# Kernel tuning notes

Hardware: AMD Instinct MI355X
Metric: run time of the kernel (lower is better)

## Reference

```python
import jax, jax.numpy as jnp
import numpy as np


def _maxpool2x2(x):
    # x: [B, C, H, W] -> [B, C, H//2, W//2], 2x2 max pool stride 2
    B, C, H, W = x.shape
    return x.reshape(B, C, H // 2, 2, W // 2, 2).max(axis=(3, 5))


def _conv1x1(w, x):
    # w: [O, I], x: [B, I, H, W] -> [B, O, H, W]
    return jnp.einsum('oi,bihw->bohw', w, x)


def setup_inputs() -> dict:
    key = jax.random.key(0)
    ks = jax.random.split(key, 5)
    B, C, H, W = 16, 64, 64, 64
    c8, c2 = C // 8, C // 2
    x = jax.random.normal(ks[0], (B, C, H, W), dtype=jnp.float32)
    # 1x1 conv weights (spectral_norm is a training-time weight reparameterization;
    # here we use the effective weights directly, scaled for stability)
    w_theta = jax.random.normal(ks[1], (c8, C), dtype=jnp.float32) / np.sqrt(C)
    w_phi = jax.random.normal(ks[2], (c8, C), dtype=jnp.float32) / np.sqrt(C)
    w_g = jax.random.normal(ks[3], (c2, C), dtype=jnp.float32) / np.sqrt(C)
    w_o = jax.random.normal(ks[4], (C, c2), dtype=jnp.float32) / np.sqrt(c2)
    gamma = jnp.ones((1,), dtype=jnp.float32)
    return {"x": x, "w_theta": w_theta, "w_phi": w_phi, "w_g": w_g, "w_o": w_o, "gamma": gamma}


def reference(x, w_theta, w_phi, w_g, w_o, gamma):
    B, C, H, W = x.shape
    c8, c2 = C // 8, C // 2
    hw, hw4 = H * W, (H * W) // 4
    theta = _conv1x1(w_theta, x).reshape(B, c8, hw)            # [B, c8, hw]
    phi = _maxpool2x2(_conv1x1(w_phi, x)).reshape(B, c8, hw4)   # [B, c8, hw/4]
    attn = jax.nn.softmax(jnp.einsum('bcq,bck->bqk', theta, phi), axis=-1)  # [B, hw, hw/4]
    g = _maxpool2x2(_conv1x1(w_g, x)).reshape(B, c2, hw4)       # [B, c2, hw/4]
    attn_g = jnp.einsum('bck,bqk->bcq', g, attn).reshape(B, c2, H, W)
    out = x + gamma * _conv1x1(w_o, attn_g)
    return out
```

## Files before the change

### kernel.cpp

```cpp
#include <hip/hip_runtime.h>
#include <hip/hip_bf16.h>

#define B_  16
#define C_  64
#define HW  4096
#define KP  1024
#define LOG2E 1.44269504088896f

typedef short short8 __attribute__((ext_vector_type(8)));
typedef float floatx16 __attribute__((ext_vector_type(16)));

union Frag { uint4 u; short8 s; };

#define G_ROW      2064
#define ATTN_ROW   144
#define UNION_SZ   73728
#define WO_OFF     UNION_SZ
#define WO_ROW     80
#define L_OFF      (WO_OFF + 5120)
#define LDS_BYTES  (L_OFF + 2048)

__device__ __forceinline__ unsigned cvt_pk_bf16(float lo, float hi) {
    unsigned r;
    asm("v_cvt_pk_bf16_f32 %0, %1, %2" : "=v"(r) : "v"(lo), "v"(hi));
    return r;
}
#define PLSWAP(a, b) asm("v_permlane32_swap_b32 %0, %1" : "+v"(a), "+v"(b))

__device__ __forceinline__ void build_pfrags(const float* p, Frag& f0, Frag& f1) {
    unsigned u0 = cvt_pk_bf16(p[0], p[1]);
    unsigned u1 = cvt_pk_bf16(p[2], p[3]);
    unsigned u2 = cvt_pk_bf16(p[4], p[5]);
    unsigned u3 = cvt_pk_bf16(p[6], p[7]);
    PLSWAP(u0, u2);
    PLSWAP(u1, u3);
    f0.u.x = u0; f0.u.y = u1; f0.u.z = u2; f0.u.w = u3;
    unsigned v0 = cvt_pk_bf16(p[8],  p[9]);
    unsigned v1 = cvt_pk_bf16(p[10], p[11]);
    unsigned v2 = cvt_pk_bf16(p[12], p[13]);
    unsigned v3 = cvt_pk_bf16(p[14], p[15]);
    PLSWAP(v0, v2);
    PLSWAP(v1, v3);
    f1.u.x = v0; f1.u.y = v1; f1.u.z = v2; f1.u.w = v3;
}

__global__ __launch_bounds__(128) void convpool_kernel(
    const float* __restrict__ x,
    const float* __restrict__ w_theta,
    const float* __restrict__ w_phi,
    const float* __restrict__ w_g,
    __hip_bfloat16* __restrict__ theta16,
    __hip_bfloat16* __restrict__ phi16,
    __hip_bfloat16* __restrict__ gT)
{
    __shared__ float conv[48 * 129];
    const int bi = blockIdx.x;
    const int b  = bi >> 5;
    const int rg = bi & 31;
    const int t  = threadIdx.x;
    const int q  = rg * 128 + t;

    const float* xp = x + (size_t)b * C_ * HW + q;

    const int lane = t & 63;
    const int ln   = lane & 31;
    const int hi   = lane >> 5;
    const int wv   = t >> 6;

    const float* wrow0 = (ln < 8)  ? (w_theta + ln * C_)
                       : (ln < 16) ? (w_phi + (ln - 8) * C_)
                                   : (w_g + (ln - 16) * C_);
    const float* wrow1 = (ln < 16) ? (w_g + (16 + ln) * C_) : (w_g + 31 * C_);

    Frag B0[4], B1[4];
    #pragma unroll
    for (int k = 0; k < 4; ++k) {
        const float* p0 = wrow0 + 16 * k + 8 * hi;
        const float4 f0 = *(const float4*)(p0);
        const float4 f1 = *(const float4*)(p0 + 4);
        B0[k].u.x = cvt_pk_bf16(f0.x, f0.y); B0[k].u.y = cvt_pk_bf16(f0.z, f0.w);
        B0[k].u.z = cvt_pk_bf16(f1.x, f1.y); B0[k].u.w = cvt_pk_bf16(f1.z, f1.w);
        const float* p1 = wrow1 + 16 * k + 8 * hi;
        const float4 g0 = *(const float4*)(p1);
        const float4 g1 = *(const float4*)(p1 + 4);
        B1[k].u.x = cvt_pk_bf16(g0.x, g0.y); B1[k].u.y = cvt_pk_bf16(g0.z, g0.w);
        B1[k].u.z = cvt_pk_bf16(g1.x, g1.y); B1[k].u.w = cvt_pk_bf16(g1.z, g1.w);
    }

    floatx16 D00 = {}, D01 = {}, D10 = {}, D11 = {};

#define CHUNK(BUF, KK)                                                          \
    {                                                                           \
        unsigned q0 = cvt_pk_bf16(BUF[0],  BUF[1]);                             \
        unsigned q1 = cvt_pk_bf16(BUF[2],  BUF[3]);                             \
        unsigned q2 = cvt_pk_bf16(BUF[4],  BUF[5]);                             \
        unsigned q3 = cvt_pk_bf16(BUF[6],  BUF[7]);                             \
        unsigned q4 = cvt_pk_bf16(BUF[8],  BUF[9]);                             \
        unsigned q5 = cvt_pk_bf16(BUF[10], BUF[11]);                            \
        unsigned q6 = cvt_pk_bf16(BUF[12], BUF[13]);                            \
        unsigned q7 = cvt_pk_bf16(BUF[14], BUF[15]);                            \
        PLSWAP(q0, q4); PLSWAP(q1, q5); PLSWAP(q2, q6); PLSWAP(q3, q7);         \
        Frag loF, hiF;                                                          \
        loF.u.x = q0; loF.u.y = q1; loF.u.z = q2; loF.u.w = q3;                 \
        hiF.u.x = q4; hiF.u.y = q5; hiF.u.z = q6; hiF.u.w = q7;                 \
        D00 = __builtin_amdgcn_mfma_f32_32x32x16_bf16(loF.s, B0[KK].s, D00, 0, 0, 0); \
        D01 = __builtin_amdgcn_mfma_f32_32x32x16_bf16(loF.s, B1[KK].s, D01, 0, 0, 0); \
        D10 = __builtin_amdgcn_mfma_f32_32x32x16_bf16(hiF.s, B0[KK].s, D10, 0, 0, 0); \
        D11 = __builtin_amdgcn_mfma_f32_32x32x16_bf16(hiF.s, B1[KK].s, D11, 0, 0, 0); \
    }

    float xa[16], xc[16];
    #pragma unroll
    for (int c = 0; c < 16; ++c) xa[c] = xp[(size_t)c * HW];
    #pragma unroll
    for (int c = 0; c < 16; ++c) xc[c] = xp[(size_t)(16 + c) * HW];
    CHUNK(xa, 0);
    #pragma unroll
    for (int c = 0; c < 16; ++c) xa[c] = xp[(size_t)(32 + c) * HW];
    CHUNK(xc, 1);
    #pragma unroll
    for (int c = 0; c < 16; ++c) xc[c] = xp[(size_t)(48 + c) * HW];
    CHUNK(xa, 2);
    CHUNK(xc, 3);
#undef CHUNK

    #pragma unroll
    for (int rI = 0; rI < 16; ++rI) {
        const int row = (rI & 3) + 8 * (rI >> 2) + 4 * hi;
        conv[ln * 129 + (wv * 64 + row)]      = D00[rI];
        conv[ln * 129 + (wv * 64 + 32 + row)] = D10[rI];
        if (ln < 16) {
            conv[(32 + ln) * 129 + (wv * 64 + row)]      = D01[rI];
            conv[(32 + ln) * 129 + (wv * 64 + 32 + row)] = D11[rI];
        }
    }
    __syncthreads();

    {
        float th[8];
        #pragma unroll
        for (int oc = 0; oc < 8; ++oc) th[oc] = conv[oc * 129 + t] * LOG2E;
        uint4 u, z = {0u, 0u, 0u, 0u};
        u.x = cvt_pk_bf16(th[0], th[1]);
        u.y = cvt_pk_bf16(th[2], th[3]);
        u.z = cvt_pk_bf16(th[4], th[5]);
        u.w = cvt_pk_bf16(th[6], th[7]);
        __hip_bfloat16* tp = theta16 + ((size_t)b * HW + q) * 16;
        *(uint4*)(tp)     = u;
        *(uint4*)(tp + 8) = z;
    }

    for (int wi = t; wi < 40 * 32; wi += 128) {
        const int oc = (wi >> 5) + 8;
        const int pc = wi & 31;
        const int i00 = pc * 2;
        const float* cp = conv + oc * 129;
        const float v = fmaxf(fmaxf(cp[i00], cp[i00 + 1]),
                              fmaxf(cp[i00 + 64], cp[i00 + 65]));
        const int kg = rg * 32 + pc;
        if (oc < 16) phi16[((size_t)b * KP + kg) * 16 + (oc - 8)] = __float2bfloat16(v);
        else         gT[((size_t)b * 32 + (oc - 16)) * KP + kg]   = __float2bfloat16(v);
    }
    if (t < 32) {
        uint4 z = {0u, 0u, 0u, 0u};
        *(uint4*)(phi16 + ((size_t)b * KP + rg * 32 + t) * 16 + 8) = z;
    }
}

__global__ __launch_bounds__(512, 2) void attn_kernel(
    const float* __restrict__ x,
    const float* __restrict__ w_o,
    const float* __restrict__ gamma_p,
    const __hip_bfloat16* __restrict__ theta16,
    const __hip_bfloat16* __restrict__ phi16,
    const __hip_bfloat16* __restrict__ gT,
    float* __restrict__ out)
{
    __shared__ __align__(16) char lds[LDS_BYTES];
    const int t = threadIdx.x;
    const int bid = (blockIdx.x & 7) * 32 + (blockIdx.x >> 3);
    const int b   = bid >> 4;
    const int qb0 = (bid & 15) * 256;

    {
        const uint4* src = (const uint4*)(gT + (size_t)b * 32 * KP);
        #pragma unroll
        for (int i = 0; i < 8; ++i) {
            const int gi = t + 512 * i;
            const int c = gi >> 7, kk = gi & 127;
            *(uint4*)(lds + c * G_ROW + kk * 16) = src[gi];
        }
    }
    if (t < 256) {
        const int co = t >> 2, part = t & 3;
        const float4* wsrc = (const float4*)(w_o + co * 32 + part * 8);
        const float4 f0 = wsrc[0], f1 = wsrc[1];
        uint4 u;
        u.x = cvt_pk_bf16(f0.x, f0.y); u.y = cvt_pk_bf16(f0.z, f0.w);
        u.z = cvt_pk_bf16(f1.x, f1.y); u.w = cvt_pk_bf16(f1.z, f1.w);
        *(uint4*)(lds + WO_OFF + co * WO_ROW + part * 16) = u;
    }
    __syncthreads();

    const int lane = t & 63;
    const int wv   = t >> 6;
    const int h    = wv >> 2;
    const int qp   = wv & 3;
    const int hi   = lane >> 5;
    const int ln   = lane & 31;
    const int qt0  = qp * 64, qt1 = qt0 + 32;
    const int kbase = h * 512;

    const uint4* thb = (const uint4*)(theta16 + ((size_t)b * HW + qb0) * 16);
    Frag bth0, bth1;
    bth0.u = thb[(qt0 + ln) * 2 + hi];
    bth1.u = thb[(qt1 + ln) * 2 + hi];

    const uint4* phb = (const uint4*)(phi16 + ((size_t)b * KP + kbase) * 16);
    const char*  gp  = lds + ln * G_ROW + kbase * 2 + hi * 16;

    floatx16 czero = {};
    floatx16 O0 = {}, O1 = {};
    float l0 = 0.f, l1 = 0.f;

    #pragma unroll 2
    for (int kb = 0; kb < 16; ++kb) {
        Frag aphi, gf0, gf1;
        aphi.u = phb[(kb * 32 + ln) * 2 + hi];
        gf0.u  = *(const uint4*)(gp + kb * 64);
        gf1.u  = *(const uint4*)(gp + kb * 64 + 32);

        floatx16 S0 = __builtin_amdgcn_mfma_f32_32x32x16_bf16(aphi.s, bth0.s, czero, 0, 0, 0);
        floatx16 S1 = __builtin_amdgcn_mfma_f32_32x32x16_bf16(aphi.s, bth1.s, czero, 0, 0, 0);

        float p0[16], p1[16];
        float la = 0.f, lb = 0.f, lc = 0.f, ld = 0.f;
        #pragma unroll
        for (int rr = 0; rr < 16; rr += 2) {
            p0[rr]   = __builtin_amdgcn_exp2f(S0[rr]);   la += p0[rr];
            p0[rr+1] = __builtin_amdgcn_exp2f(S0[rr+1]); lb += p0[rr+1];
        }
        #pragma unroll
        for (int rr = 0; rr < 16; rr += 2) {
            p1[rr]   = __builtin_amdgcn_exp2f(S1[rr]);   lc += p1[rr];
            p1[rr+1] = __builtin_amdgcn_exp2f(S1[rr+1]); ld += p1[rr+1];
        }
        l0 += la + lb; l1 += lc + ld;

        Frag pa00, pa01, pa10, pa11;
        build_pfrags(p0, pa00, pa01);
        build_pfrags(p1, pa10, pa11);

        O0 = __builtin_amdgcn_mfma_f32_32x32x16_bf16(pa00.s, gf0.s, O0, 0, 0, 0);
        O0 = __builtin_amdgcn_mfma_f32_32x32x16_bf16(pa01.s, gf1.s, O0, 0, 0, 0);
        O1 = __builtin_amdgcn_mfma_f32_32x32x16_bf16(pa10.s, gf0.s, O1, 0, 0, 0);
        O1 = __builtin_amdgcn_mfma_f32_32x32x16_bf16(pa11.s, gf1.s, O1, 0, 0, 0);
    }

    __syncthreads();

    #pragma unroll
    for (int rr = 0; rr < 16; ++rr) {
        const int rm = (rr & 3) + 8 * (rr >> 2) + 4 * hi;
        *(float*)(lds + ((h << 8) + qt0 + rm) * ATTN_ROW + ln * 4) = O0[rr];
        *(float*)(lds + ((h << 8) + qt1 + rm) * ATTN_ROW + ln * 4) = O1[rr];
    }
    const float l0t = l0 + __shfl_xor(l0, 32, 64);
    const float l1t = l1 + __shfl_xor(l1, 32, 64);
    {
        const int   lq = hi ? (qt1 + ln) : (qt0 + ln);
        const float lw = hi ? l1t : l0t;
        *(float*)(lds + L_OFF + ((h << 8) + lq) * 4) = lw;
    }
    __syncthreads();

    const float gam = gamma_p[0];
    const int   qt  = wv * 32;
    const float lt  = *(const float*)(lds + L_OFF + (qt + ln) * 4)
                    + *(const float*)(lds + L_OFF + (256 + qt + ln) * 4);
    const float gl  = gam / lt;

    const char* ab0 = lds + (qt + ln) * ATTN_ROW + hi * 32;
    const char* ab1 = ab0 + 256 * ATTN_ROW;
    float4 a0 = *(const float4*)(ab0);
    float4 a1 = *(const float4*)(ab0 + 16);
    float4 a2 = *(const float4*)(ab0 + 64);
    float4 a3 = *(const float4*)(ab0 + 80);
    const float4 c0 = *(const float4*)(ab1);
    const float4 c1 = *(const float4*)(ab1 + 16);
    const float4 c2 = *(const float4*)(ab1 + 64);
    const float4 c3 = *(const float4*)(ab1 + 80);
    a0.x += c0.x; a0.y += c0.y; a0.z += c0.z; a0.w += c0.w;
    a1.x += c1.x; a1.y += c1.y; a1.z += c1.z; a1.w += c1.w;
    a2.x += c2.x; a2.y += c2.y; a2.z += c2.z; a2.w += c2.w;
    a3.x += c3.x; a3.y += c3.y; a3.z += c3.z; a3.w += c3.w;

    Frag bat0, bat1;
    bat0.u.x = cvt_pk_bf16(a0.x, a0.y); bat0.u.y = cvt_pk_bf16(a0.z, a0.w);
    bat0.u.z = cvt_pk_bf16(a1.x, a1.y); bat0.u.w = cvt_pk_bf16(a1.z, a1.w);
    bat1.u.x = cvt_pk_bf16(a2.x, a2.y); bat1.u.y = cvt_pk_bf16(a2.z, a2.w);
    bat1.u.z = cvt_pk_bf16(a3.x, a3.y); bat1.u.w = cvt_pk_bf16(a3.z, a3.w);

    const char* wb = lds + WO_OFF + ln * WO_ROW + hi * 16;
    Frag wa00, wa01, wa10, wa11;
    wa00.u = *(const uint4*)(wb);
    wa01.u = *(const uint4*)(wb + 32);
    wa10.u = *(const uint4*)(wb + 32 * WO_ROW);
    wa11.u = *(const uint4*)(wb + 32 * WO_ROW + 32);

    floatx16 D0 = __builtin_amdgcn_mfma_f32_32x32x16_bf16(wa00.s, bat0.s, czero, 0, 0, 0);
    D0 = __builtin_amdgcn_mfma_f32_32x32x16_bf16(wa01.s, bat1.s, D0, 0, 0, 0);
    floatx16 D1 = __builtin_amdgcn_mfma_f32_32x32x16_bf16(wa10.s, bat0.s, czero, 0, 0, 0);
    D1 = __builtin_amdgcn_mfma_f32_32x32x16_bf16(wa11.s, bat1.s, D1, 0, 0, 0);

    const int qg = qb0 + qt + ln;
    const float* xb = x   + (size_t)b * C_ * HW + qg;
    float*       ob = out + (size_t)b * C_ * HW + qg;
    #pragma unroll
    for (int rr = 0; rr < 16; ++rr) {
        const int co = (rr & 3) + 8 * (rr >> 2) + 4 * hi;
        ob[(size_t)co * HW]        = xb[(size_t)co * HW]        + gl * D0[rr];
        ob[(size_t)(co + 32) * HW] = xb[(size_t)(co + 32) * HW] + gl * D1[rr];
    }
}

extern "C" void kernel_launch(void* const* d_in, const int* in_sizes, int n_in,
                              void* d_out, int out_size, void* d_ws, size_t ws_size,
                              hipStream_t stream) {
    const float* x       = (const float*)d_in[0];
    const float* w_theta = (const float*)d_in[1];
    const float* w_phi   = (const float*)d_in[2];
    const float* w_g     = (const float*)d_in[3];
    const float* w_o     = (const float*)d_in[4];
    const float* gamma   = (const float*)d_in[5];
    float* out = (float*)d_out;

    __hip_bfloat16* theta16 = (__hip_bfloat16*)d_ws;
    __hip_bfloat16* phi16   = theta16 + (size_t)B_ * HW * 16;
    __hip_bfloat16* gT      = phi16   + (size_t)B_ * KP * 16;

    convpool_kernel<<<dim3(B_ * 32), dim3(128), 0, stream>>>(
        x, w_theta, w_phi, w_g, theta16, phi16, gT);
    attn_kernel<<<dim3(B_ * 16), dim3(512), 0, stream>>>(
        x, w_o, gamma, theta16, phi16, gT, out);
}
```

Baseline: 31.45 us.

## Split conv input channels across waves and shrink attention tiles for more blocks

The conv kernel now uses 256 threads, stages x tiles through LDS with coalesced float4 loads, and splits the 64 input channels between two wave halves, summing the partial results in LDS. The attention kernel moves from 256 blocks of 512 threads handling 256 queries each to 1024 blocks of 256 threads handling 64 queries each. It reads g directly from global memory instead of staging it in LDS and stages theta in LDS. The aim is higher occupancy and better load balance across the CUs, at the cost of redundant phi/g reads per block and an output epilogue that only half the waves run.

```diff
diff --git a/kernel.cpp b/kernel.cpp
--- a/kernel.cpp
+++ b/kernel.cpp
@@ -11,14 +11,6 @@
 typedef float floatx16 __attribute__((ext_vector_type(16)));
 
 union Frag { uint4 u; short8 s; };
-
-#define G_ROW      2064
-#define ATTN_ROW   144
-#define UNION_SZ   73728
-#define WO_OFF     UNION_SZ
-#define WO_ROW     80
-#define L_OFF      (WO_OFF + 5120)
-#define LDS_BYTES  (L_OFF + 2048)
 
 __device__ __forceinline__ unsigned cvt_pk_bf16(float lo, float hi) {
     unsigned r;
@@ -44,7 +36,12 @@
     f1.u.x = v0; f1.u.y = v1; f1.u.z = v2; f1.u.w = v3;
 }
 
-__global__ __launch_bounds__(128) void convpool_kernel(
+#define XS_ROW   528
+#define CV_ROW2  532
+#define CV_HALF  25536
+#define CLDS_SZ  51072
+
+__global__ __launch_bounds__(256) void convpool_kernel(
     const float* __restrict__ x,
     const float* __restrict__ w_theta,
     const float* __restrict__ w_phi,
@@ -53,110 +50,121 @@
     __hip_bfloat16* __restrict__ phi16,
     __hip_bfloat16* __restrict__ gT)
 {
-    __shared__ float conv[48 * 129];
+    __shared__ __align__(16) char clds[CLDS_SZ];
     const int bi = blockIdx.x;
     const int b  = bi >> 5;
     const int rg = bi & 31;
     const int t  = threadIdx.x;
-    const int q  = rg * 128 + t;
-
-    const float* xp = x + (size_t)b * C_ * HW + q;
 
     const int lane = t & 63;
     const int ln   = lane & 31;
     const int hi   = lane >> 5;
     const int wv   = t >> 6;
+    const int half = wv >> 1;
+    const int pt   = wv & 1;
+
+    {
+        const float* xsrc = x + (size_t)b * C_ * HW + rg * 128;
+        #pragma unroll
+        for (int i = 0; i < 8; ++i) {
+            const int idx = t + 256 * i;
+            const int c = idx >> 5, p4 = (idx & 31) * 4;
+            const float4 v = *(const float4*)(xsrc + (size_t)c * HW + p4);
+            *(float4*)(clds + c * XS_ROW + p4 * 4) = v;
+        }
+    }
 
     const float* wrow0 = (ln < 8)  ? (w_theta + ln * C_)
                        : (ln < 16) ? (w_phi + (ln - 8) * C_)
                                    : (w_g + (ln - 16) * C_);
     const float* wrow1 = (ln < 16) ? (w_g + (16 + ln) * C_) : (w_g + 31 * C_);
-
-    Frag B0[4], B1[4];
+    Frag B0[2], B1[2];
     #pragma unroll
-    for (int k = 0; k < 4; ++k) {
-        const float* p0 = wrow0 + 16 * k + 8 * hi;
+    for (int k = 0; k < 2; ++k) {
+        const float* p0 = wrow0 + 32 * half + 16 * k + 8 * hi;
         const float4 f0 = *(const float4*)(p0);
         const float4 f1 = *(const float4*)(p0 + 4);
         B0[k].u.x = cvt_pk_bf16(f0.x, f0.y); B0[k].u.y = cvt_pk_bf16(f0.z, f0.w);
         B0[k].u.z = cvt_pk_bf16(f1.x, f1.y); B0[k].u.w = cvt_pk_bf16(f1.z, f1.w);
-        const float* p1 = wrow1 + 16 * k + 8 * hi;
+        const float* p1 = wrow1 + 32 * half + 16 * k + 8 * hi;
         const float4 g0 = *(const float4*)(p1);
         const float4 g1 = *(const float4*)(p1 + 4);
         B1[k].u.x = cvt_pk_bf16(g0.x, g0.y); B1[k].u.y = cvt_pk_bf16(g0.z, g0.w);
         B1[k].u.z = cvt_pk_bf16(g1.x, g1.y); B1[k].u.w = cvt_pk_bf16(g1.z, g1.w);
     }
+    __syncthreads();
+
+    const int px = pt * 64 + lane;
+    Frag AL[2], AH[2];
+    #pragma unroll
+    for (int k = 0; k < 2; ++k) {
+        float v[16];
+        #pragma unroll
+        for (int j = 0; j < 16; ++j)
+            v[j] = *(const float*)(clds + (32 * half + 16 * k + j) * XS_ROW + px * 4);
+        unsigned q0 = cvt_pk_bf16(v[0],  v[1]);
+        unsigned q1 = cvt_pk_bf16(v[2],  v[3]);
+        unsigned q2 = cvt_pk_bf16(v[4],  v[5]);
+        unsigned q3 = cvt_pk_bf16(v[6],  v[7]);
+        unsigned q4 = cvt_pk_bf16(v[8],  v[9]);
+        unsigned q5 = cvt_pk_bf16(v[10], v[11]);
+        unsigned q6 = cvt_pk_bf16(v[12], v[13]);
+        unsigned q7 = cvt_pk_bf16(v[14], v[15]);
+        PLSWAP(q0, q4); PLSWAP(q1, q5); PLSWAP(q2, q6); PLSWAP(q3, q7);
+        AL[k].u.x = q0; AL[k].u.y = q1; AL[k].u.z = q2; AL[k].u.w = q3;
+        AH[k].u.x = q4; AH[k].u.y = q5; AH[k].u.z = q6; AH[k].u.w = q7;
+    }
+    __syncthreads();
 
     floatx16 D00 = {}, D01 = {}, D10 = {}, D11 = {};
-
-#define CHUNK(BUF, KK)                                                          \
-    {                                                                           \
-        unsigned q0 = cvt_pk_bf16(BUF[0],  BUF[1]);                             \
-        unsigned q1 = cvt_pk_bf16(BUF[2],  BUF[3]);                             \
-        unsigned q2 = cvt_pk_bf16(BUF[4],  BUF[5]);                             \
-        unsigned q3 = cvt_pk_bf16(BUF[6],  BUF[7]);                             \
-        unsigned q4 = cvt_pk_bf16(BUF[8],  BUF[9]);                             \
-        unsigned q5 = cvt_pk_bf16(BUF[10], BUF[11]);                            \
-        unsigned q6 = cvt_pk_bf16(BUF[12], BUF[13]);                            \
-        unsigned q7 = cvt_pk_bf16(BUF[14], BUF[15]);                            \
-        PLSWAP(q0, q4); PLSWAP(q1, q5); PLSWAP(q2, q6); PLSWAP(q3, q7);         \
-        Frag loF, hiF;                                                          \
-        loF.u.x = q0; loF.u.y = q1; loF.u.z = q2; loF.u.w = q3;                 \
-        hiF.u.x = q4; hiF.u.y = q5; hiF.u.z = q6; hiF.u.w = q7;                 \
-        D00 = __builtin_amdgcn_mfma_f32_32x32x16_bf16(loF.s, B0[KK].s, D00, 0, 0, 0); \
-        D01 = __builtin_amdgcn_mfma_f32_32x32x16_bf16(loF.s, B1[KK].s, D01, 0, 0, 0); \
-        D10 = __builtin_amdgcn_mfma_f32_32x32x16_bf16(hiF.s, B0[KK].s, D10, 0, 0, 0); \
-        D11 = __builtin_amdgcn_mfma_f32_32x32x16_bf16(hiF.s, B1[KK].s, D11, 0, 0, 0); \
-    }
-
-    float xa[16], xc[16];
     #pragma unroll
-    for (int c = 0; c < 16; ++c) xa[c] = xp[(size_t)c * HW];
-    #pragma unroll
-    for (int c = 0; c < 16; ++c) xc[c] = xp[(size_t)(16 + c) * HW];
-    CHUNK(xa, 0);
-    #pragma unroll
-    for (int c = 0; c < 16; ++c) xa[c] = xp[(size_t)(32 + c) * HW];
-    CHUNK(xc, 1);
-    #pragma unroll
-    for (int c = 0; c < 16; ++c) xc[c] = xp[(size_t)(48 + c) * HW];
-    CHUNK(xa, 2);
-    CHUNK(xc, 3);
-#undef CHUNK
-
-    #pragma unroll
-    for (int rI = 0; rI < 16; ++rI) {
-        const int row = (rI & 3) + 8 * (rI >> 2) + 4 * hi;
-        conv[ln * 129 + (wv * 64 + row)]      = D00[rI];
-        conv[ln * 129 + (wv * 64 + 32 + row)] = D10[rI];
-        if (ln < 16) {
-            conv[(32 + ln) * 129 + (wv * 64 + row)]      = D01[rI];
-            conv[(32 + ln) * 129 + (wv * 64 + 32 + row)] = D11[rI];
+    for (int k = 0; k < 2; ++k) {
+        D00 = __builtin_amdgcn_mfma_f32_32x32x16_bf16(AL[k].s, B0[k].s, D00, 0, 0, 0);
+        D01 = __builtin_amdgcn_mfma_f32_32x32x16_bf16(AL[k].s, B1[k].s, D01, 0, 0, 0);
+        D10 = __builtin_amdgcn_mfma_f32_32x32x16_bf16(AH[k].s, B0[k].s, D10, 0, 0, 0);
+        D11 = __builtin_amdgcn_mfma_f32_32x32x16_bf16(AH[k].s, B1[k].s, D11, 0, 0, 0);
+    }
+
+    {
+        char* base = clds + half * CV_HALF;
+        #pragma unroll
+        for (int r = 0; r < 16; ++r) {
+            const int row = (r & 3) + 8 * (r >> 2) + 4 * hi;
+            *(float*)(base + ln * CV_ROW2 + (pt * 64 + row) * 4)      = D00[r];
+            *(float*)(base + ln * CV_ROW2 + (pt * 64 + 32 + row) * 4) = D10[r];
+            if (ln < 16) {
+                *(float*)(base + (32 + ln) * CV_ROW2 + (pt * 64 + row) * 4)      = D01[r];
+                *(float*)(base + (32 + ln) * CV_ROW2 + (pt * 64 + 32 + row) * 4) = D11[r];
+            }
         }
     }
     __syncthreads();
 
-    {
+    if (t < 128) {
         float th[8];
         #pragma unroll
-        for (int oc = 0; oc < 8; ++oc) th[oc] = conv[oc * 129 + t] * LOG2E;
-        uint4 u, z = {0u, 0u, 0u, 0u};
-        u.x = cvt_pk_bf16(th[0], th[1]);
-        u.y = cvt_pk_bf16(th[2], th[3]);
-        u.z = cvt_pk_bf16(th[4], th[5]);
-        u.w = cvt_pk_bf16(th[6], th[7]);
-        __hip_bfloat16* tp = theta16 + ((size_t)b * HW + q) * 16;
+        for (int oc = 0; oc < 8; ++oc)
+            th[oc] = (*(const float*)(clds + oc * CV_ROW2 + t * 4)
+                    + *(const float*)(clds + CV_HALF + oc * CV_ROW2 + t * 4)) * LOG2E;
+        uint4 u; uint4 z = {0u, 0u, 0u, 0u};
+        u.x = cvt_pk_bf16(th[0], th[1]); u.y = cvt_pk_bf16(th[2], th[3]);
+        u.z = cvt_pk_bf16(th[4], th[5]); u.w = cvt_pk_bf16(th[6], th[7]);
+        __hip_bfloat16* tp = theta16 + ((size_t)b * HW + rg * 128 + t) * 16;
         *(uint4*)(tp)     = u;
         *(uint4*)(tp + 8) = z;
     }
 
-    for (int wi = t; wi < 40 * 32; wi += 128) {
+    for (int wi = t; wi < 1280; wi += 256) {
         const int oc = (wi >> 5) + 8;
         const int pc = wi & 31;
-        const int i00 = pc * 2;
-        const float* cp = conv + oc * 129;
-        const float v = fmaxf(fmaxf(cp[i00], cp[i00 + 1]),
-                              fmaxf(cp[i00 + 64], cp[i00 + 65]));
+        const char* c0 = clds + oc * CV_ROW2;
+        const char* c1 = clds + CV_HALF + oc * CV_ROW2;
+        const int i0 = pc * 8;
+        const float v00 = *(const float*)(c0 + i0)       + *(const float*)(c1 + i0);
+        const float v01 = *(const float*)(c0 + i0 + 4)   + *(const float*)(c1 + i0 + 4);
+        const float v10 = *(const float*)(c0 + i0 + 256) + *(const float*)(c1 + i0 + 256);
+        const float v11 = *(const float*)(c0 + i0 + 260) + *(const float*)(c1 + i0 + 260);
+        const float v = fmaxf(fmaxf(v00, v01), fmaxf(v10, v11));
         const int kg = rg * 32 + pc;
         if (oc < 16) phi16[((size_t)b * KP + kg) * 16 + (oc - 8)] = __float2bfloat16(v);
         else         gT[((size_t)b * 32 + (oc - 16)) * KP + kg]   = __float2bfloat16(v);
@@ -167,7 +175,15 @@
     }
 }
 
-__global__ __launch_bounds__(512, 2) void attn_kernel(
+#define AT_OFF   0
+#define AT_ROW   144
+#define AL_OFF   18432
+#define TH2_OFF  18944
+#define WO2_OFF  20992
+#define WO_ROW   80
+#define ALDS_SZ  26112
+
+__global__ __launch_bounds__(256, 4) void attn_kernel(
     const float* __restrict__ x,
     const float* __restrict__ w_o,
     const float* __restrict__ gamma_p,
@@ -176,52 +192,45 @@
     const __hip_bfloat16* __restrict__ gT,
     float* __restrict__ out)
 {
-    __shared__ __align__(16) char lds[LDS_BYTES];
+    __shared__ __align__(16) char lds[ALDS_SZ];
     const int t = threadIdx.x;
-    const int bid = (blockIdx.x & 7) * 32 + (blockIdx.x >> 3);
-    const int b   = bid >> 4;
-    const int qb0 = (bid & 15) * 256;
-
+    const int xcd = blockIdx.x & 7, slot = blockIdx.x >> 3;
+    const int b   = xcd * 2 + (slot >> 6);
+    const int qb0 = (slot & 63) * 64;
+
+    if (t < 128) {
+        const uint4* src = (const uint4*)(theta16 + ((size_t)b * HW + qb0) * 16);
+        ((uint4*)(lds + TH2_OFF))[t] = src[t];
+    }
     {
-        const uint4* src = (const uint4*)(gT + (size_t)b * 32 * KP);
-        #pragma unroll
-        for (int i = 0; i < 8; ++i) {
-            const int gi = t + 512 * i;
-            const int c = gi >> 7, kk = gi & 127;
-            *(uint4*)(lds + c * G_ROW + kk * 16) = src[gi];
-        }
-    }
-    if (t < 256) {
         const int co = t >> 2, part = t & 3;
         const float4* wsrc = (const float4*)(w_o + co * 32 + part * 8);
         const float4 f0 = wsrc[0], f1 = wsrc[1];
         uint4 u;
         u.x = cvt_pk_bf16(f0.x, f0.y); u.y = cvt_pk_bf16(f0.z, f0.w);
         u.z = cvt_pk_bf16(f1.x, f1.y); u.w = cvt_pk_bf16(f1.z, f1.w);
-        *(uint4*)(lds + WO_OFF + co * WO_ROW + part * 16) = u;
+        *(uint4*)(lds + WO2_OFF + co * WO_ROW + part * 16) = u;
     }
     __syncthreads();
 
     const int lane = t & 63;
+    const int ln   = lane & 31;
+    const int hi   = lane >> 5;
     const int wv   = t >> 6;
-    const int h    = wv >> 2;
-    const int qp   = wv & 3;
-    const int hi   = lane >> 5;
-    const int ln   = lane & 31;
-    const int qt0  = qp * 64, qt1 = qt0 + 32;
-    const int kbase = h * 512;
-
-    const uint4* thb = (const uint4*)(theta16 + ((size_t)b * HW + qb0) * 16);
-    Frag bth0, bth1;
-    bth0.u = thb[(qt0 + ln) * 2 + hi];
-    bth1.u = thb[(qt1 + ln) * 2 + hi];
+    const int kh   = wv >> 1;
+    const int qp   = wv & 1;
+    const int qt   = qp * 32;
+    const int kbase = kh * 512;
+
+    Frag bth;
+    bth.u = *(const uint4*)(lds + TH2_OFF + (qt + ln) * 32 + hi * 16);
 
     const uint4* phb = (const uint4*)(phi16 + ((size_t)b * KP + kbase) * 16);
-    const char*  gp  = lds + ln * G_ROW + kbase * 2 + hi * 16;
+    const char*  gp  = (const char*)gT + ((size_t)(b * 32 + ln) * KP + kbase) * 2 + hi * 16;
 
     floatx16 czero = {};
-    floatx16 O0 = {}, O1 = {};
-    float l0 = 0.f, l1 = 0.f;
+    floatx16 O = {};
+    float l = 0.f;
 
     #pragma unroll 2
     for (int kb = 0; kb < 16; ++kb) {
@@ -230,97 +239,82 @@
         gf0.u  = *(const uint4*)(gp + kb * 64);
         gf1.u  = *(const uint4*)(gp + kb * 64 + 32);
 
-        floatx16 S0 = __builtin_amdgcn_mfma_f32_32x32x16_bf16(aphi.s, bth0.s, czero, 0, 0, 0);
-        floatx16 S1 = __builtin_amdgcn_mfma_f32_32x32x16_bf16(aphi.s, bth1.s, czero, 0, 0, 0);
-
-        float p0[16], p1[16];
-        float la = 0.f, lb = 0.f, lc = 0.f, ld = 0.f;
+        floatx16 S = __builtin_amdgcn_mfma_f32_32x32x16_bf16(aphi.s, bth.s, czero, 0, 0, 0);
+
+        float p[16];
+        float la = 0.f, lb = 0.f;
         #pragma unroll
         for (int rr = 0; rr < 16; rr += 2) {
-            p0[rr]   = __builtin_amdgcn_exp2f(S0[rr]);   la += p0[rr];
-            p0[rr+1] = __builtin_amdgcn_exp2f(S0[rr+1]); lb += p0[rr+1];
+            p[rr]   = __builtin_amdgcn_exp2f(S[rr]);   la += p[rr];
+            p[rr+1] = __builtin_amdgcn_exp2f(S[rr+1]); lb += p[rr+1];
         }
-        #pragma unroll
-        for (int rr = 0; rr < 16; rr += 2) {
-            p1[rr]   = __builtin_amdgcn_exp2f(S1[rr]);   lc += p1[rr];
-            p1[rr+1] = __builtin_amdgcn_exp2f(S1[rr+1]); ld += p1[rr+1];
-        }
-        l0 += la + lb; l1 += lc + ld;
-
-        Frag pa00, pa01, pa10, pa11;
-        build_pfrags(p0, pa00, pa01);
-        build_pfrags(p1, pa10, pa11);
-
-        O0 = __builtin_amdgcn_mfma_f32_32x32x16_bf16(pa00.s, gf0.s, O0, 0, 0, 0);
-        O0 = __builtin_amdgcn_mfma_f32_32x32x16_bf16(pa01.s, gf1.s, O0, 0, 0, 0);
-        O1 = __builtin_amdgcn_mfma_f32_32x32x16_bf16(pa10.s, gf0.s, O1, 0, 0, 0);
-        O1 = __builtin_amdgcn_mfma_f32_32x32x16_bf16(pa11.s, gf1.s, O1, 0, 0, 0);
-    }
-
-    __syncthreads();
+        l += la + lb;
+
+        Frag pa0, pa1;
+        build_pfrags(p, pa0, pa1);
+        O = __builtin_amdgcn_mfma_f32_32x32x16_bf16(pa0.s, gf0.s, O, 0, 0, 0);
+        O = __builtin_amdgcn_mfma_f32_32x32x16_bf16(pa1.s, gf1.s, O, 0, 0, 0);
+    }
 
     #pragma unroll
     for (int rr = 0; rr < 16; ++rr) {
         const int rm = (rr & 3) + 8 * (rr >> 2) + 4 * hi;
-        *(float*)(lds + ((h << 8) + qt0 + rm) * ATTN_ROW + ln * 4) = O0[rr];
-        *(float*)(lds + ((h << 8) + qt1 + rm) * ATTN_ROW + ln * 4) = O1[rr];
-    }
-    const float l0t = l0 + __shfl_xor(l0, 32, 64);
-    const float l1t = l1 + __shfl_xor(l1, 32, 64);
-    {
-        const int   lq = hi ? (qt1 + ln) : (qt0 + ln);
-        const float lw = hi ? l1t : l0t;
-        *(float*)(lds + L_OFF + ((h << 8) + lq) * 4) = lw;
-    }
-    __syncthreads();
-
-    const float gam = gamma_p[0];
-    const int   qt  = wv * 32;
-    const float lt  = *(const float*)(lds + L_OFF + (qt + ln) * 4)
-                    + *(const float*)(lds + L_OFF + (256 + qt + ln) * 4);
-    const float gl  = gam / lt;
-
-    const char* ab0 = lds + (qt + ln) * ATTN_ROW + hi * 32;
-    const char* ab1 = ab0 + 256 * ATTN_ROW;
-    float4 a0 = *(const float4*)(ab0);
-    float4 a1 = *(const float4*)(ab0 + 16);
-    float4 a2 = *(const float4*)(ab0 + 64);
-    float4 a3 = *(const float4*)(ab0 + 80);
-    const float4 c0 = *(const float4*)(ab1);
-    const float4 c1 = *(const float4*)(ab1 + 16);
-    const float4 c2 = *(const float4*)(ab1 + 64);
-    const float4 c3 = *(const float4*)(ab1 + 80);
-    a0.x += c0.x; a0.y += c0.y; a0.z += c0.z; a0.w += c0.w;
-    a1.x += c1.x; a1.y += c1.y; a1.z += c1.z; a1.w += c1.w;
-    a2.x += c2.x; a2.y += c2.y; a2.z += c2.z; a2.w += c2.w;
-    a3.x += c3.x; a3.y += c3.y; a3.z += c3.z; a3.w += c3.w;
-
-    Frag bat0, bat1;
-    bat0.u.x = cvt_pk_bf16(a0.x, a0.y); bat0.u.y = cvt_pk_bf16(a0.z, a0.w);
-    bat0.u.z = cvt_pk_bf16(a1.x, a1.y); bat0.u.w = cvt_pk_bf16(a1.z, a1.w);
-    bat1.u.x = cvt_pk_bf16(a2.x, a2.y); bat1.u.y = cvt_pk_bf16(a2.z, a2.w);
-    bat1.u.z = cvt_pk_bf16(a3.x, a3.y); bat1.u.w = cvt_pk_bf16(a3.z, a3.w);
-
-    const char* wb = lds + WO_OFF + ln * WO_ROW + hi * 16;
-    Frag wa00, wa01, wa10, wa11;
-    wa00.u = *(const uint4*)(wb);
-    wa01.u = *(const uint4*)(wb + 32);
-    wa10.u = *(const uint4*)(wb + 32 * WO_ROW);
-    wa11.u = *(const uint4*)(wb + 32 * WO_ROW + 32);
-
-    floatx16 D0 = __builtin_amdgcn_mfma_f32_32x32x16_bf16(wa00.s, bat0.s, czero, 0, 0, 0);
-    D0 = __builtin_amdgcn_mfma_f32_32x32x16_bf16(wa01.s, bat1.s, D0, 0, 0, 0);
-    floatx16 D1 = __builtin_amdgcn_mfma_f32_32x32x16_bf16(wa10.s, bat0.s, czero, 0, 0, 0);
-    D1 = __builtin_amdgcn_mfma_f32_32x32x16_bf16(wa11.s, bat1.s, D1, 0, 0, 0);
-
-    const int qg = qb0 + qt + ln;
-    const float* xb = x   + (size_t)b * C_ * HW + qg;
-    float*       ob = out + (size_t)b * C_ * HW + qg;
-    #pragma unroll
-    for (int rr = 0; rr < 16; ++rr) {
-        const int co = (rr & 3) + 8 * (rr >> 2) + 4 * hi;
-        ob[(size_t)co * HW]        = xb[(size_t)co * HW]        + gl * D0[rr];
-        ob[(size_t)(co + 32) * HW] = xb[(size_t)(co + 32) * HW] + gl * D1[rr];
+        *(float*)(lds + AT_OFF + (kh * 64 + qt + rm) * AT_ROW + ln * 4) = O[rr];
+    }
+    const float lt2 = l + __shfl_xor(l, 32, 64);
+    if (hi == 0)
+        *(float*)(lds + AL_OFF + (kh * 64 + qt + ln) * 4) = lt2;
+    __syncthreads();
+
+    if (wv < 2) {
+        const int   qtile = wv * 32;
+        const float gam = gamma_p[0];
+        const float lt = *(const float*)(lds + AL_OFF + (qtile + ln) * 4)
+                       + *(const float*)(lds + AL_OFF + (64 + qtile + ln) * 4);
+        const float gl = gam / lt;
+
+        const char* ab0 = lds + AT_OFF + (qtile + ln) * AT_ROW + hi * 32;
+        const char* ab1 = ab0 + 64 * AT_ROW;
+        float4 a0 = *(const float4*)(ab0);
+        float4 a1 = *(const float4*)(ab0 + 16);
+        float4 a2 = *(const float4*)(ab0 + 64);
+        float4 a3 = *(const float4*)(ab0 + 80);
+        const float4 c0 = *(const float4*)(ab1);
+        const float4 c1 = *(const float4*)(ab1 + 16);
+        const float4 c2 = *(const float4*)(ab1 + 64);
+        const float4 c3 = *(const float4*)(ab1 + 80);
+        a0.x += c0.x; a0.y += c0.y; a0.z += c0.z; a0.w += c0.w;
+        a1.x += c1.x; a1.y += c1.y; a1.z += c1.z; a1.w += c1.w;
+        a2.x += c2.x; a2.y += c2.y; a2.z += c2.z; a2.w += c2.w;
+        a3.x += c3.x; a3.y += c3.y; a3.z += c3.z; a3.w += c3.w;
+
+        Frag bat0, bat1;
+        bat0.u.x = cvt_pk_bf16(a0.x, a0.y); bat0.u.y = cvt_pk_bf16(a0.z, a0.w);
+        bat0.u.z = cvt_pk_bf16(a1.x, a1.y); bat0.u.w = cvt_pk_bf16(a1.z, a1.w);
+        bat1.u.x = cvt_pk_bf16(a2.x, a2.y); bat1.u.y = cvt_pk_bf16(a2.z, a2.w);
+        bat1.u.z = cvt_pk_bf16(a3.x, a3.y); bat1.u.w = cvt_pk_bf16(a3.z, a3.w);
+
+        const char* wb = lds + WO2_OFF + ln * WO_ROW + hi * 16;
+        Frag wa00, wa01, wa10, wa11;
+        wa00.u = *(const uint4*)(wb);
+        wa01.u = *(const uint4*)(wb + 32);
+        wa10.u = *(const uint4*)(wb + 32 * WO_ROW);
+        wa11.u = *(const uint4*)(wb + 32 * WO_ROW + 32);
+
+        floatx16 D0 = __builtin_amdgcn_mfma_f32_32x32x16_bf16(wa00.s, bat0.s, czero, 0, 0, 0);
+        D0 = __builtin_amdgcn_mfma_f32_32x32x16_bf16(wa01.s, bat1.s, D0, 0, 0, 0);
+        floatx16 D1 = __builtin_amdgcn_mfma_f32_32x32x16_bf16(wa10.s, bat0.s, czero, 0, 0, 0);
+        D1 = __builtin_amdgcn_mfma_f32_32x32x16_bf16(wa11.s, bat1.s, D1, 0, 0, 0);
+
+        const int qg = qb0 + qtile + ln;
+        const float* xb = x   + (size_t)b * C_ * HW + qg;
+        float*       ob = out + (size_t)b * C_ * HW + qg;
+        #pragma unroll
+        for (int rr = 0; rr < 16; ++rr) {
+            const int co = (rr & 3) + 8 * (rr >> 2) + 4 * hi;
+            ob[(size_t)co * HW]        = xb[(size_t)co * HW]        + gl * D0[rr];
+            ob[(size_t)(co + 32) * HW] = xb[(size_t)(co + 32) * HW] + gl * D1[rr];
+        }
     }
 }
 
@@ -339,8 +333,8 @@
     __hip_bfloat16* phi16   = theta16 + (size_t)B_ * HW * 16;
     __hip_bfloat16* gT      = phi16   + (size_t)B_ * KP * 16;
 
-    convpool_kernel<<<dim3(B_ * 32), dim3(128), 0, stream>>>(
+    convpool_kernel<<<dim3(B_ * 32), dim3(256), 0, stream>>>(
         x, w_theta, w_phi, w_g, theta16, phi16, gT);
-    attn_kernel<<<dim3(B_ * 16), dim3(512), 0, stream>>>(
+    attn_kernel<<<dim3(B_ * 64), dim3(256), 0, stream>>>(
         x, w_o, gamma, theta16, phi16, gT, out);
 }
```

Result: slower. 35.07 us (+11.5%).
